# Kernel tuning notes

Hardware: AMD Instinct MI355X
Metric: run time of the kernel (lower is better)

Reference implementation:

```python
import jax, jax.numpy as jnp
import numpy as np

EPS = 1e-3  # keras LayerNormalization default epsilon


def layer_norm(x, gamma, beta):
    mean = jnp.mean(x, axis=-1, keepdims=True)
    var = jnp.var(x, axis=-1, keepdims=True)
    return (x - mean) * jax.lax.rsqrt(var + EPS) * gamma + beta


def setup_inputs() -> dict:
    key = jax.random.key(0)
    ks = jax.random.split(key, 4)
    B, H, W, C, Ci = 16, 64, 64, 512, 64
    return {
        "x": jax.random.normal(ks[0], (B, H, W, C), dtype=jnp.float32),
        "Wf": jax.random.normal(ks[1], (C, Ci), dtype=jnp.float32) * (1.0 / np.sqrt(C)),
        "Wh": jax.random.normal(ks[2], (C, Ci), dtype=jnp.float32) * (1.0 / np.sqrt(C)),
        "Wfgh": jax.random.normal(ks[3], (Ci, C), dtype=jnp.float32) * (1.0 / np.sqrt(Ci)),
        "gamma_f": jnp.ones((Ci,), jnp.float32),
        "beta_f": jnp.zeros((Ci,), jnp.float32),
        "gamma_h": jnp.ones((Ci,), jnp.float32),
        "beta_h": jnp.zeros((Ci,), jnp.float32),
        "gamma_fgh": jnp.ones((C,), jnp.float32),
        "beta_fgh": jnp.zeros((C,), jnp.float32),
        "scale": jnp.ones((1,), jnp.float32),
    }


def reference(x, Wf, Wh, Wfgh, gamma_f, beta_f, gamma_h, beta_h, gamma_fgh, beta_fgh, scale):
    # NOTE: original code uses w_f / LN_f for BOTH f and g branches (w_g unused).
    fg_base = layer_norm(jnp.einsum("bhwc,cd->bhwd", x, Wf), gamma_f, beta_f)  # [B,H,W,Ci]
    f = jnp.transpose(fg_base, (0, 2, 1, 3))  # Permute(2,1,3): swap H and W
    g = fg_base
    h = layer_norm(jnp.einsum("bhwc,cd->bhwd", x, Wh), gamma_h, beta_h)
    attn = jax.nn.softmax(f * g, axis=1)  # softmax over height axis
    out = jnp.einsum("bhwd,dc->bhwc", attn * h, Wfgh)
    out = layer_norm(out, gamma_fgh, beta_fgh)
    return out * scale + x
```

## Files before the change

### kernel.cpp

```cpp
#include <hip/hip_runtime.h>
#include <math.h>

#define BB 16
#define HH 64
#define WW 64
#define CC 512
#define CI 64
#define NROWS (BB * HH * WW)
#define LN_EPS 1e-3f

typedef __attribute__((ext_vector_type(8))) short bf16x8;
typedef __attribute__((ext_vector_type(4))) float f32x4;

__device__ __forceinline__ unsigned short f2bf(float f) {
  union {
    float f;
    unsigned int u;
  } v;
  v.f = f;
  unsigned int r = v.u + 0x7FFF + ((v.u >> 16) & 1);
  return (unsigned short)(r >> 16);
}

__device__ __forceinline__ float bf2f(unsigned short u) {
  union {
    unsigned int u;
    float f;
  } v;
  v.u = ((unsigned int)u) << 16;
  return v.f;
}

__global__ __launch_bounds__(256) void sgsa_prep(
    const float* __restrict__ Wf, const float* __restrict__ Wh,
    const float* __restrict__ Wo, unsigned short* __restrict__ WcT,
    unsigned short* __restrict__ WoT) {
  int tid = blockIdx.x * 256 + threadIdx.x;
  for (int i = tid; i < 128 * 512; i += gridDim.x * 256) {
    int col = i >> 9, k = i & 511;
    float v = (col < 64) ? Wf[k * 64 + col] : Wh[k * 64 + (col - 64)];
    WcT[i] = f2bf(v);
  }
  for (int i = tid; i < 512 * 64; i += gridDim.x * 256) {
    int col = i >> 6, k = i & 63;
    WoT[i] = f2bf(Wo[k * 512 + col]);
  }
}

__global__ __launch_bounds__(256) void sgsa_k1_mfma(
    const float* __restrict__ x, const unsigned short* __restrict__ WcT,
    const float* __restrict__ gf, const float* __restrict__ bf,
    const float* __restrict__ gh, const float* __restrict__ bh,
    float* __restrict__ fg, float* __restrict__ hl) {
  const int lane = threadIdx.x & 63;
  const int wid = blockIdx.x * 4 + (threadIdx.x >> 6);
  const int row0 = wid * 32;
  const int cq = lane & 15;
  const int kg = lane >> 4;

  f32x4 acc[2][8];
#pragma unroll
  for (int rt = 0; rt < 2; ++rt)
#pragma unroll
    for (int ct = 0; ct < 8; ++ct) acc[rt][ct] = (f32x4){0.f, 0.f, 0.f, 0.f};

  for (int kk = 0; kk < 16; ++kk) {
    const int kb = kk * 32 + kg * 8;
    bf16x8 bfr[8];
#pragma unroll
    for (int ct = 0; ct < 8; ++ct) {
      const int col = ct * 16 + cq;
      bfr[ct] = *(const bf16x8*)&WcT[col * 512 + kb];
    }
#pragma unroll
    for (int rt = 0; rt < 2; ++rt) {
      const float* ap = &x[(size_t)(row0 + rt * 16 + cq) * CC + kb];
      f32x4 a0 = *(const f32x4*)ap;
      f32x4 a1 = *(const f32x4*)(ap + 4);
      bf16x8 af;
#pragma unroll
      for (int j = 0; j < 4; ++j) {
        af[j] = (short)f2bf(a0[j]);
        af[j + 4] = (short)f2bf(a1[j]);
      }
#pragma unroll
      for (int ct = 0; ct < 8; ++ct)
        acc[rt][ct] = __builtin_amdgcn_mfma_f32_16x16x32_bf16(
            af, bfr[ct], acc[rt][ct], 0, 0, 0);
    }
  }

  float gfv[4], bfv[4], ghv[4], bhv[4];
#pragma unroll
  for (int ct = 0; ct < 4; ++ct) {
    gfv[ct] = gf[ct * 16 + cq];
    bfv[ct] = bf[ct * 16 + cq];
    ghv[ct] = gh[ct * 16 + cq];
    bhv[ct] = bh[ct * 16 + cq];
  }

#pragma unroll
  for (int rt = 0; rt < 2; ++rt) {
#pragma unroll
    for (int r = 0; r < 4; ++r) {
      const int row = row0 + rt * 16 + kg * 4 + r;
      float s = acc[rt][0][r] + acc[rt][1][r] + acc[rt][2][r] + acc[rt][3][r];
      float q = acc[rt][0][r] * acc[rt][0][r] + acc[rt][1][r] * acc[rt][1][r] +
                acc[rt][2][r] * acc[rt][2][r] + acc[rt][3][r] * acc[rt][3][r];
#pragma unroll
      for (int m = 1; m < 16; m <<= 1) {
        s += __shfl_xor(s, m, 64);
        q += __shfl_xor(q, m, 64);
      }
      float mean = s * (1.f / 64.f);
      float var = q * (1.f / 64.f) - mean * mean;
      float inv = rsqrtf(var + LN_EPS);
#pragma unroll
      for (int ct = 0; ct < 4; ++ct) {
        float v = (acc[rt][ct][r] - mean) * inv * gfv[ct] + bfv[ct];
        fg[(size_t)row * CI + ct * 16 + cq] = v;
      }
      float s2 = acc[rt][4][r] + acc[rt][5][r] + acc[rt][6][r] + acc[rt][7][r];
      float q2 = acc[rt][4][r] * acc[rt][4][r] + acc[rt][5][r] * acc[rt][5][r] +
                 acc[rt][6][r] * acc[rt][6][r] + acc[rt][7][r] * acc[rt][7][r];
#pragma unroll
      for (int m = 1; m < 16; m <<= 1) {
        s2 += __shfl_xor(s2, m, 64);
        q2 += __shfl_xor(q2, m, 64);
      }
      float mean2 = s2 * (1.f / 64.f);
      float var2 = q2 * (1.f / 64.f) - mean2 * mean2;
      float inv2 = rsqrtf(var2 + LN_EPS);
#pragma unroll
      for (int ct = 0; ct < 4; ++ct) {
        float v = (acc[rt][ct + 4][r] - mean2) * inv2 * ghv[ct] + bhv[ct];
        hl[(size_t)row * CI + ct * 16 + cq] = v;
      }
    }
  }
}

__global__ __launch_bounds__(256) void sgsa_k2_softmax(
    const float* __restrict__ fg, float* __restrict__ hl) {
  const int bw = blockIdx.x;
  const int b = bw >> 6;
  const int w = bw & 63;
  const int d = threadIdx.x & 63;
  const int q = threadIdx.x >> 6;

  float sv[16], hv[16];
#pragma unroll
  for (int i = 0; i < 16; ++i) {
    int h = q * 16 + i;
    float g = fg[(size_t)(((b * 64 + h) * 64 + w) * 64) + d];
    float f = fg[(size_t)(((b * 64 + w) * 64 + h) * 64) + d];
    sv[i] = f * g;
    hv[i] = hl[(size_t)(((b * 64 + h) * 64 + w) * 64) + d];
  }

  __shared__ float red[4][64];

  float m = sv[0];
#pragma unroll
  for (int i = 1; i < 16; ++i) m = fmaxf(m, sv[i]);
  red[q][d] = m;
  __syncthreads();
  m = fmaxf(fmaxf(red[0][d], red[1][d]), fmaxf(red[2][d], red[3][d]));
  __syncthreads();

  float ssum = 0.f;
#pragma unroll
  for (int i = 0; i < 16; ++i) {
    sv[i] = __expf(sv[i] - m);
    ssum += sv[i];
  }
  red[q][d] = ssum;
  __syncthreads();
  ssum = (red[0][d] + red[1][d]) + (red[2][d] + red[3][d]);
  float rinv = 1.f / ssum;

#pragma unroll
  for (int i = 0; i < 16; ++i) {
    int h = q * 16 + i;
    hl[(size_t)(((b * 64 + h) * 64 + w) * 64) + d] = sv[i] * rinv * hv[i];
  }
}

__global__ __launch_bounds__(256) void sgsa_k3_mfma(
    const float* __restrict__ t, const unsigned short* __restrict__ WoT,
    const float* __restrict__ go, const float* __restrict__ bo,
    const float* __restrict__ scale, const float* __restrict__ x,
    float* __restrict__ out) {
  const int lane = threadIdx.x & 63;
  const int wv = threadIdx.x >> 6;
  const int row0 = blockIdx.x * 32;
  const int col0 = wv * 128;
  const int cq = lane & 15;
  const int kg = lane >> 4;

  f32x4 acc[2][8];
#pragma unroll
  for (int rt = 0; rt < 2; ++rt)
#pragma unroll
    for (int ct = 0; ct < 8; ++ct) acc[rt][ct] = (f32x4){0.f, 0.f, 0.f, 0.f};

#pragma unroll
  for (int kk = 0; kk < 2; ++kk) {
    const int kb = kk * 32 + kg * 8;
    bf16x8 bfr[8];
#pragma unroll
    for (int ct = 0; ct < 8; ++ct) {
      const int col = col0 + ct * 16 + cq;
      bfr[ct] = *(const bf16x8*)&WoT[col * CI + kb];
    }
#pragma unroll
    for (int rt = 0; rt < 2; ++rt) {
      const float* ap = &t[(size_t)(row0 + rt * 16 + cq) * CI + kb];
      f32x4 a0 = *(const f32x4*)ap;
      f32x4 a1 = *(const f32x4*)(ap + 4);
      bf16x8 ah, al;
#pragma unroll
      for (int j = 0; j < 4; ++j) {
        unsigned short h0 = f2bf(a0[j]);
        unsigned short h1 = f2bf(a1[j]);
        ah[j] = (short)h0;
        ah[j + 4] = (short)h1;
        al[j] = (short)f2bf(a0[j] - bf2f(h0));
        al[j + 4] = (short)f2bf(a1[j] - bf2f(h1));
      }
#pragma unroll
      for (int ct = 0; ct < 8; ++ct) {
        acc[rt][ct] = __builtin_amdgcn_mfma_f32_16x16x32_bf16(
            ah, bfr[ct], acc[rt][ct], 0, 0, 0);
        acc[rt][ct] = __builtin_amdgcn_mfma_f32_16x16x32_bf16(
            al, bfr[ct], acc[rt][ct], 0, 0, 0);
      }
    }
  }

  __shared__ float s_red[4][32];
  __shared__ float q_red[4][32];

  float svv[2][4], qvv[2][4];
#pragma unroll
  for (int rt = 0; rt < 2; ++rt) {
#pragma unroll
    for (int r = 0; r < 4; ++r) {
      float s = 0.f, q = 0.f;
#pragma unroll
      for (int ct = 0; ct < 8; ++ct) {
        float v = acc[rt][ct][r];
        s += v;
        q += v * v;
      }
#pragma unroll
      for (int m = 1; m < 16; m <<= 1) {
        s += __shfl_xor(s, m, 64);
        q += __shfl_xor(q, m, 64);
      }
      svv[rt][r] = s;
      qvv[rt][r] = q;
      if (cq == 0) {
        s_red[wv][rt * 16 + kg * 4 + r] = s;
        q_red[wv][rt * 16 + kg * 4 + r] = q;
      }
    }
  }
  __syncthreads();

  const float sc = scale[0];
  float gov[8], bov[8];
#pragma unroll
  for (int ct = 0; ct < 8; ++ct) {
    gov[ct] = go[col0 + ct * 16 + cq];
    bov[ct] = bo[col0 + ct * 16 + cq];
  }

#pragma unroll
  for (int rt = 0; rt < 2; ++rt) {
#pragma unroll
    for (int r = 0; r < 4; ++r) {
      const int ridx = rt * 16 + kg * 4 + r;
      const int row = row0 + ridx;
      float s = (s_red[0][ridx] + s_red[1][ridx]) +
                (s_red[2][ridx] + s_red[3][ridx]);
      float q = (q_red[0][ridx] + q_red[1][ridx]) +
                (q_red[2][ridx] + q_red[3][ridx]);
      float mean = s * (1.f / 512.f);
      float var = q * (1.f / 512.f) - mean * mean;
      float inv = rsqrtf(var + LN_EPS);
      const size_t base = (size_t)row * CC;
#pragma unroll
      for (int ct = 0; ct < 8; ++ct) {
        const int col = col0 + ct * 16 + cq;
        float o = (acc[rt][ct][r] - mean) * inv * gov[ct] + bov[ct];
        out[base + col] = o * sc + x[base + col];
      }
    }
  }
}

extern "C" void kernel_launch(void* const* d_in, const int* in_sizes, int n_in,
                              void* d_out, int out_size, void* d_ws,
                              size_t ws_size, hipStream_t stream) {
  const float* x = (const float*)d_in[0];
  const float* Wf = (const float*)d_in[1];
  const float* Wh = (const float*)d_in[2];
  const float* Wo = (const float*)d_in[3];
  const float* gf = (const float*)d_in[4];
  const float* bf = (const float*)d_in[5];
  const float* gh = (const float*)d_in[6];
  const float* bh = (const float*)d_in[7];
  const float* go = (const float*)d_in[8];
  const float* bo = (const float*)d_in[9];
  const float* sc = (const float*)d_in[10];
  float* out = (float*)d_out;

  unsigned short* WcT = (unsigned short*)d_ws;
  unsigned short* WoT = WcT + 128 * 512;
  float* fg = (float*)((char*)d_ws + (256 << 10));
  float* hl = fg + (size_t)NROWS * CI;

  sgsa_prep<<<64, 256, 0, stream>>>(Wf, Wh, Wo, WcT, WoT);
  sgsa_k1_mfma<<<NROWS / 128, 256, 0, stream>>>(x, WcT, gf, bf, gh, bh, fg,
                                                hl);
  sgsa_k2_softmax<<<BB * WW, 256, 0, stream>>>(fg, hl);
  sgsa_k3_mfma<<<NROWS / 32, 256, 0, stream>>>(hl, WoT, go, bo, sc, x, out);
}
```

Measured before the change: 133.2 us.

## Fuse height-softmax with output projection GEMM via shared-memory bf16 split

Merges the softmax kernel and the output MFMA GEMM + LayerNorm + residual kernel into one kernel, one block per (batch, width) column. The attention-weighted values are stored as hi/lo bf16 pairs in LDS and fed straight to the MFMA loop, so the fp32 intermediate no longer makes a round trip through global memory and one launch is removed. In exchange there are only 1024 blocks, each with a larger accumulator tile (4x8 MFMA tiles per wave), which raises register pressure and limits occupancy. Output rows are also written with a large stride between heights. It also adds an unroll-2 pragma on the first GEMM's K loop and doubles the prep kernel's grid.

```diff
diff --git a/kernel.cpp b/kernel.cpp
--- a/kernel.cpp
+++ b/kernel.cpp
@@ -64,6 +64,7 @@
 #pragma unroll
     for (int ct = 0; ct < 8; ++ct) acc[rt][ct] = (f32x4){0.f, 0.f, 0.f, 0.f};
 
+#pragma unroll 2
   for (int kk = 0; kk < 16; ++kk) {
     const int kb = kk * 32 + kg * 8;
     bf16x8 bfr[8];
@@ -140,67 +141,76 @@
   }
 }
 
-__global__ __launch_bounds__(256) void sgsa_k2_softmax(
-    const float* __restrict__ fg, float* __restrict__ hl) {
-  const int bw = blockIdx.x;
-  const int b = bw >> 6;
-  const int w = bw & 63;
-  const int d = threadIdx.x & 63;
-  const int q = threadIdx.x >> 6;
-
-  float sv[16], hv[16];
-#pragma unroll
-  for (int i = 0; i < 16; ++i) {
-    int h = q * 16 + i;
-    float g = fg[(size_t)(((b * 64 + h) * 64 + w) * 64) + d];
-    float f = fg[(size_t)(((b * 64 + w) * 64 + h) * 64) + d];
-    sv[i] = f * g;
-    hv[i] = hl[(size_t)(((b * 64 + h) * 64 + w) * 64) + d];
-  }
-
+__global__ __launch_bounds__(256) void sgsa_k23(
+    const float* __restrict__ fg, const float* __restrict__ hl,
+    const unsigned short* __restrict__ WoT, const float* __restrict__ go,
+    const float* __restrict__ bo, const float* __restrict__ scale,
+    const float* __restrict__ x, float* __restrict__ out) {
+  const int b = blockIdx.x >> 6;
+  const int w = blockIdx.x & 63;
+  const int tid = threadIdx.x;
+
+  __shared__ unsigned short t_hi[64 * 72];
+  __shared__ unsigned short t_lo[64 * 72];
   __shared__ float red[4][64];
-
-  float m = sv[0];
-#pragma unroll
-  for (int i = 1; i < 16; ++i) m = fmaxf(m, sv[i]);
-  red[q][d] = m;
+  __shared__ float s_red[4][64];
+  __shared__ float q_red[4][64];
+
+  {
+    const int d = tid & 63;
+    const int q = tid >> 6;
+    const size_t base_g = (size_t)((b * 64) * 64 + w) * 64;
+    const size_t base_f = (size_t)((b * 64 + w) * 64) * 64;
+
+    float sv[16], hv[16];
+#pragma unroll
+    for (int i = 0; i < 16; ++i) {
+      int h = q * 16 + i;
+      float g = fg[base_g + (size_t)h * 4096 + d];
+      float f = fg[base_f + (size_t)h * 64 + d];
+      sv[i] = f * g;
+      hv[i] = hl[base_g + (size_t)h * 4096 + d];
+    }
+
+    float m = sv[0];
+#pragma unroll
+    for (int i = 1; i < 16; ++i) m = fmaxf(m, sv[i]);
+    red[q][d] = m;
+    __syncthreads();
+    m = fmaxf(fmaxf(red[0][d], red[1][d]), fmaxf(red[2][d], red[3][d]));
+    __syncthreads();
+
+    float ssum = 0.f;
+#pragma unroll
+    for (int i = 0; i < 16; ++i) {
+      sv[i] = __expf(sv[i] - m);
+      ssum += sv[i];
+    }
+    red[q][d] = ssum;
+    __syncthreads();
+    ssum = (red[0][d] + red[1][d]) + (red[2][d] + red[3][d]);
+    float rinv = 1.f / ssum;
+
+#pragma unroll
+    for (int i = 0; i < 16; ++i) {
+      int h = q * 16 + i;
+      float t = sv[i] * rinv * hv[i];
+      unsigned short th = f2bf(t);
+      t_hi[h * 72 + d] = th;
+      t_lo[h * 72 + d] = f2bf(t - bf2f(th));
+    }
+  }
   __syncthreads();
-  m = fmaxf(fmaxf(red[0][d], red[1][d]), fmaxf(red[2][d], red[3][d]));
-  __syncthreads();
-
-  float ssum = 0.f;
-#pragma unroll
-  for (int i = 0; i < 16; ++i) {
-    sv[i] = __expf(sv[i] - m);
-    ssum += sv[i];
-  }
-  red[q][d] = ssum;
-  __syncthreads();
-  ssum = (red[0][d] + red[1][d]) + (red[2][d] + red[3][d]);
-  float rinv = 1.f / ssum;
-
-#pragma unroll
-  for (int i = 0; i < 16; ++i) {
-    int h = q * 16 + i;
-    hl[(size_t)(((b * 64 + h) * 64 + w) * 64) + d] = sv[i] * rinv * hv[i];
-  }
-}
-
-__global__ __launch_bounds__(256) void sgsa_k3_mfma(
-    const float* __restrict__ t, const unsigned short* __restrict__ WoT,
-    const float* __restrict__ go, const float* __restrict__ bo,
-    const float* __restrict__ scale, const float* __restrict__ x,
-    float* __restrict__ out) {
-  const int lane = threadIdx.x & 63;
-  const int wv = threadIdx.x >> 6;
-  const int row0 = blockIdx.x * 32;
+
+  const int lane = tid & 63;
+  const int wv = tid >> 6;
   const int col0 = wv * 128;
   const int cq = lane & 15;
   const int kg = lane >> 4;
 
-  f32x4 acc[2][8];
-#pragma unroll
-  for (int rt = 0; rt < 2; ++rt)
+  f32x4 acc[4][8];
+#pragma unroll
+  for (int rt = 0; rt < 4; ++rt)
 #pragma unroll
     for (int ct = 0; ct < 8; ++ct) acc[rt][ct] = (f32x4){0.f, 0.f, 0.f, 0.f};
 
@@ -214,20 +224,9 @@
       bfr[ct] = *(const bf16x8*)&WoT[col * CI + kb];
     }
 #pragma unroll
-    for (int rt = 0; rt < 2; ++rt) {
-      const float* ap = &t[(size_t)(row0 + rt * 16 + cq) * CI + kb];
-      f32x4 a0 = *(const f32x4*)ap;
-      f32x4 a1 = *(const f32x4*)(ap + 4);
-      bf16x8 ah, al;
-#pragma unroll
-      for (int j = 0; j < 4; ++j) {
-        unsigned short h0 = f2bf(a0[j]);
-        unsigned short h1 = f2bf(a1[j]);
-        ah[j] = (short)h0;
-        ah[j + 4] = (short)h1;
-        al[j] = (short)f2bf(a0[j] - bf2f(h0));
-        al[j + 4] = (short)f2bf(a1[j] - bf2f(h1));
-      }
+    for (int rt = 0; rt < 4; ++rt) {
+      bf16x8 ah = *(const bf16x8*)&t_hi[(rt * 16 + cq) * 72 + kb];
+      bf16x8 al = *(const bf16x8*)&t_lo[(rt * 16 + cq) * 72 + kb];
 #pragma unroll
       for (int ct = 0; ct < 8; ++ct) {
         acc[rt][ct] = __builtin_amdgcn_mfma_f32_16x16x32_bf16(
@@ -238,31 +237,25 @@
     }
   }
 
-  __shared__ float s_red[4][32];
-  __shared__ float q_red[4][32];
-
-  float svv[2][4], qvv[2][4];
-#pragma unroll
-  for (int rt = 0; rt < 2; ++rt) {
+#pragma unroll
+  for (int rt = 0; rt < 4; ++rt) {
 #pragma unroll
     for (int r = 0; r < 4; ++r) {
-      float s = 0.f, q = 0.f;
+      float s = 0.f, qq = 0.f;
 #pragma unroll
       for (int ct = 0; ct < 8; ++ct) {
         float v = acc[rt][ct][r];
         s += v;
-        q += v * v;
+        qq += v * v;
       }
 #pragma unroll
       for (int m = 1; m < 16; m <<= 1) {
         s += __shfl_xor(s, m, 64);
-        q += __shfl_xor(q, m, 64);
-      }
-      svv[rt][r] = s;
-      qvv[rt][r] = q;
+        qq += __shfl_xor(qq, m, 64);
+      }
       if (cq == 0) {
         s_red[wv][rt * 16 + kg * 4 + r] = s;
-        q_red[wv][rt * 16 + kg * 4 + r] = q;
+        q_red[wv][rt * 16 + kg * 4 + r] = qq;
       }
     }
   }
@@ -277,19 +270,16 @@
   }
 
 #pragma unroll
-  for (int rt = 0; rt < 2; ++rt) {
+  for (int rt = 0; rt < 4; ++rt) {
 #pragma unroll
     for (int r = 0; r < 4; ++r) {
-      const int ridx = rt * 16 + kg * 4 + r;
-      const int row = row0 + ridx;
-      float s = (s_red[0][ridx] + s_red[1][ridx]) +
-                (s_red[2][ridx] + s_red[3][ridx]);
-      float q = (q_red[0][ridx] + q_red[1][ridx]) +
-                (q_red[2][ridx] + q_red[3][ridx]);
+      const int h = rt * 16 + kg * 4 + r;
+      float s = (s_red[0][h] + s_red[1][h]) + (s_red[2][h] + s_red[3][h]);
+      float q = (q_red[0][h] + q_red[1][h]) + (q_red[2][h] + q_red[3][h]);
       float mean = s * (1.f / 512.f);
       float var = q * (1.f / 512.f) - mean * mean;
       float inv = rsqrtf(var + LN_EPS);
-      const size_t base = (size_t)row * CC;
+      const size_t base = (size_t)((b * 64 + h) * 64 + w) * CC;
 #pragma unroll
       for (int ct = 0; ct < 8; ++ct) {
         const int col = col0 + ct * 16 + cq;
@@ -321,9 +311,8 @@
   float* fg = (float*)((char*)d_ws + (256 << 10));
   float* hl = fg + (size_t)NROWS * CI;
 
-  sgsa_prep<<<64, 256, 0, stream>>>(Wf, Wh, Wo, WcT, WoT);
+  sgsa_prep<<<128, 256, 0, stream>>>(Wf, Wh, Wo, WcT, WoT);
   sgsa_k1_mfma<<<NROWS / 128, 256, 0, stream>>>(x, WcT, gf, bf, gh, bh, fg,
                                                 hl);
-  sgsa_k2_softmax<<<BB * WW, 256, 0, stream>>>(fg, hl);
-  sgsa_k3_mfma<<<NROWS / 32, 256, 0, stream>>>(hl, WoT, go, bo, sc, x, out);
-}
+  sgsa_k23<<<BB * WW, 256, 0, stream>>>(fg, hl, WoT, go, bo, sc, x, out);
+}
```

After: 136.5 us. 1.02x slower.
